# Kernel optimization log

Hardware: AMD Instinct MI355X
Metric: run time of the kernel (lower is better)

## Reference

```python
import jax, jax.numpy as jnp
import numpy as np

B, T, C, H, E, K = 8, 1024, 768, 12, 8, 2
HS = C // H          # head_size = 64
F = 4 * C            # expert hidden = 3072
DE, SE = 2, 6        # 2 'deep' experts, 6 'simple' experts (i<2 -> deep)
LN_EPS = 1e-5
TEMP_LO, TEMP_HI = 0.5, 2.0


def setup_inputs() -> dict:
    key = jax.random.key(0)
    ks = jax.random.split(key, 20)
    n = lambda k, s, sc=0.02: (jax.random.normal(k, s, dtype=jnp.float32) * sc)
    return {
        "x": jax.random.normal(ks[0], (B, T, C), dtype=jnp.float32),
        "router_noise": jax.random.normal(ks[1], (B, T, E), dtype=jnp.float32),
        # attention params (heads stacked on leading axis)
        "wq": n(ks[2], (H, C, HS)), "wk": n(ks[3], (H, C, HS)), "wv": n(ks[4], (H, C, HS)),
        "w_proj": n(ks[5], (C, C)), "b_proj": jnp.zeros((C,), jnp.float32),
        "ln1_g": jnp.ones((C,), jnp.float32), "ln1_b": jnp.zeros((C,), jnp.float32),
        "ln2_g": jnp.ones((C,), jnp.float32), "ln2_b": jnp.zeros((C,), jnp.float32),
        # router (bias init -3.0 per source)
        "w_route": n(ks[6], (C, E)), "b_route": jnp.full((E,), -3.0, jnp.float32),
        "w_noise": n(ks[7], (C, E)), "b_noise": jnp.zeros((E,), jnp.float32),
        "temperature": jnp.float32(0.8),
        # deep experts: Linear(C,4C)-GELU-Linear(4C,4C)-GELU-Linear(4C,C), residual LayerNorm
        "deep_w1": n(ks[8], (DE, C, F)), "deep_b1": jnp.zeros((DE, F), jnp.float32),
        "deep_w2": n(ks[9], (DE, F, F)), "deep_b2": jnp.zeros((DE, F), jnp.float32),
        "deep_w3": n(ks[10], (DE, F, C)), "deep_b3": jnp.zeros((DE, C), jnp.float32),
        "deep_ln_g": jnp.ones((DE, C), jnp.float32), "deep_ln_b": jnp.zeros((DE, C), jnp.float32),
        # simple experts: Linear(C,4C)-GELU-Linear(4C,C), residual LayerNorm
        "simple_w1": n(ks[11], (SE, C, F)), "simple_b1": jnp.zeros((SE, F), jnp.float32),
        "simple_w2": n(ks[12], (SE, F, C)), "simple_b2": jnp.zeros((SE, C), jnp.float32),
        "simple_ln_g": jnp.ones((SE, C), jnp.float32), "simple_ln_b": jnp.zeros((SE, C), jnp.float32),
    }


def _ln(x, g, b):
    m = jnp.mean(x, axis=-1, keepdims=True)
    v = jnp.mean((x - m) ** 2, axis=-1, keepdims=True)
    return (x - m) * jax.lax.rsqrt(v + LN_EPS) * g + b


def reference(x, router_noise, wq, wk, wv, w_proj, b_proj, ln1_g, ln1_b, ln2_g, ln2_b,
              w_route, b_route, w_noise, b_noise, temperature,
              deep_w1, deep_b1, deep_w2, deep_b2, deep_w3, deep_b3, deep_ln_g, deep_ln_b,
              simple_w1, simple_b1, simple_w2, simple_b2, simple_ln_g, simple_ln_b):
    gelu = lambda z: jax.nn.gelu(z, approximate=False)  # torch nn.GELU default = exact erf

    # ---- multi-head causal self-attention (scale = C**-0.5, full embed dim, per source) ----
    h = _ln(x, ln1_g, ln1_b)
    q = jnp.einsum('btc,hcd->bhtd', h, wq)
    k = jnp.einsum('btc,hcd->bhtd', h, wk)
    v = jnp.einsum('btc,hcd->bhtd', h, wv)
    scores = jnp.einsum('bhtd,bhsd->bhts', q, k) * (C ** -0.5)
    causal = jnp.tril(jnp.ones((T, T), dtype=bool))
    scores = jnp.where(causal, scores, -jnp.inf)
    attn = jax.nn.softmax(scores, axis=-1)
    o = jnp.einsum('bhts,bhsd->bthd', attn, v).reshape(B, T, C)
    x = x + (o @ w_proj + b_proj)

    # ---- noisy top-k router ----
    h2 = _ln(x, ln2_g, ln2_b)
    logits = h2 @ w_route + b_route                       # [B,T,E]
    noise_scale = jax.nn.softplus(h2 @ w_noise + b_noise)
    temp = jnp.clip(temperature, TEMP_LO, TEMP_HI)
    noisy = logits + temp * router_noise * noise_scale
    _, idx = jax.lax.top_k(noisy, K)                      # [B,T,K]
    mask = jnp.sum(jax.nn.one_hot(idx, E, dtype=jnp.float32), axis=-2) > 0
    gate = jax.nn.softmax(jnp.where(mask, noisy, -jnp.inf), axis=-1)  # sparse gating [B,T,E]

    # ---- dense all-expert evaluation (as in source) + gated combine ----
    N = B * T
    hf = h2.reshape(N, C)
    # deep experts (indices 0..DE-1)
    d = gelu(jnp.einsum('nc,ecf->nef', hf, deep_w1) + deep_b1)
    d = gelu(jnp.einsum('nef,efg->neg', d, deep_w2) + deep_b2)
    d = jnp.einsum('nef,efc->nec', d, deep_w3) + deep_b3
    deep_out = _ln(hf[:, None, :] + d, deep_ln_g, deep_ln_b)          # [N,DE,C]
    # simple experts (indices DE..E-1)
    s = gelu(jnp.einsum('nc,ecf->nef', hf, simple_w1) + simple_b1)
    s = jnp.einsum('nef,efc->nec', s, simple_w2) + simple_b2
    simple_out = _ln(hf[:, None, :] + s, simple_ln_g, simple_ln_b)    # [N,SE,C]

    out_all = jnp.concatenate([deep_out, simple_out], axis=1)         # [N,E,C]
    final = jnp.einsum('nec,ne->nc', out_all, gate.reshape(N, E))
    return x + final.reshape(B, T, C)
```

## Files before the change

### kernel.cpp

```cpp
#include <hip/hip_runtime.h>
#include <cstdint>
#include <cstddef>
#include <math.h>

typedef uint16_t u16;
typedef __attribute__((ext_vector_type(8))) short short8;
typedef __attribute__((ext_vector_type(4))) float f32x4;

#define TOK 8192
#define CDIM 768
#define FDIM 3072

#define GLDS16(g, l) __builtin_amdgcn_global_load_lds((const __attribute__((address_space(1))) uint32_t*)(g), (__attribute__((address_space(3))) uint32_t*)(l), 16, 0, 0)

__device__ __forceinline__ u16 f2bf(float f) {
  union { float f; uint32_t u; } v; v.f = f;
  uint32_t u = v.u;
  return (u16)((u + 0x7FFFu + ((u >> 16) & 1u)) >> 16);
}

__device__ __forceinline__ void split2(float y, u16& hi, u16& lo) {
  u16 h = f2bf(y);
  union { uint32_t u; float f; } hf; hf.u = ((uint32_t)h) << 16;
  hi = h;
  lo = f2bf(y - hf.f);
}

__device__ __forceinline__ float gelu_exact(float z) {
  return 0.5f * z * (1.0f + erff(z * 0.70710678118654752f));
}

__device__ __forceinline__ float softplus_f(float x) {
  return (x > 0.0f) ? (x + log1pf(expf(-x))) : log1pf(expf(x));
}

__device__ __forceinline__ float block_sum256(float v, float* sm) {
  #pragma unroll
  for (int m = 1; m < 64; m <<= 1) v += __shfl_xor(v, m);
  int w = threadIdx.x >> 6;
  if ((threadIdx.x & 63) == 0) sm[w] = v;
  __syncthreads();
  v = sm[0] + sm[1] + sm[2] + sm[3];
  __syncthreads();
  return v;
}


__global__ __launch_bounds__(256) void pack_qkv(const float* __restrict__ wq,
    const float* __restrict__ wk, const float* __restrict__ wv, float* __restrict__ W) {
  int id = blockIdx.x * 256 + threadIdx.x;
  if (id >= 768 * 2304) return;
  int c = id / 2304, j = id - c * 2304;
  int which = j / 768, jj = j - which * 768;
  int hh = jj >> 6, d = jj & 63;
  const float* src = (which == 0) ? wq : (which == 1 ? wk : wv);
  W[id] = src[((size_t)hh * 768 + c) * 64 + d];
}

__global__ __launch_bounds__(256) void transpose_cast(const float* __restrict__ src,
    u16* __restrict__ dst, int K, int N) {
  __shared__ float t[32][33];
  size_t eoff = (size_t)blockIdx.z * K * N;
  const float* S = src + eoff;
  u16* D = dst + eoff;
  int n0 = blockIdx.x * 32, k0 = blockIdx.y * 32;
  int tc = threadIdx.x & 31, tr = threadIdx.x >> 5;
  #pragma unroll
  for (int r = tr; r < 32; r += 8) t[r][tc] = S[(size_t)(k0 + r) * N + n0 + tc];
  __syncthreads();
  #pragma unroll
  for (int r = tr; r < 32; r += 8) D[(size_t)(n0 + r) * K + k0 + tc] = f2bf(t[tc][r]);
}

__global__ __launch_bounds__(256) void transpose_split_k(const float* __restrict__ src,
    u16* __restrict__ Dhi, u16* __restrict__ Dlo, int K, int N) {
  __shared__ float t[32][33];
  int n0 = blockIdx.x * 32, k0 = blockIdx.y * 32;
  int tc = threadIdx.x & 31, tr = threadIdx.x >> 5;
  #pragma unroll
  for (int r = tr; r < 32; r += 8) t[r][tc] = src[(size_t)(k0 + r) * N + n0 + tc];
  __syncthreads();
  #pragma unroll
  for (int r = tr; r < 32; r += 8) {
    u16 hi, lo;
    split2(t[tc][r], hi, lo);
    size_t o = (size_t)(n0 + r) * K + k0 + tc;
    Dhi[o] = hi; Dlo[o] = lo;
  }
}


__global__ __launch_bounds__(256) void ln1_split_k(const float* __restrict__ X,
    const float* __restrict__ g, const float* __restrict__ b,
    u16* __restrict__ Yhi, u16* __restrict__ Ylo) {
  __shared__ float sm[4];
  size_t row = blockIdx.x;
  const float* x = X + row * 768;
  int t = threadIdx.x;
  float v0 = x[t], v1 = x[t + 256], v2 = x[t + 512];
  float mean = block_sum256(v0 + v1 + v2, sm) * (1.0f / 768.0f);
  float d0 = v0 - mean, d1 = v1 - mean, d2 = v2 - mean;
  float var = block_sum256(d0 * d0 + d1 * d1 + d2 * d2, sm) * (1.0f / 768.0f);
  float rstd = 1.0f / sqrtf(var + 1e-5f);
  float y0 = d0 * rstd * g[t]       + b[t];
  float y1 = d1 * rstd * g[t + 256] + b[t + 256];
  float y2 = d2 * rstd * g[t + 512] + b[t + 512];
  u16 h, lo;
  split2(y0, h, lo); Yhi[row * 768 + t]       = h; Ylo[row * 768 + t]       = lo;
  split2(y1, h, lo); Yhi[row * 768 + t + 256] = h; Ylo[row * 768 + t + 256] = lo;
  split2(y2, h, lo); Yhi[row * 768 + t + 512] = h; Ylo[row * 768 + t + 512] = lo;
}

__global__ __launch_bounds__(256) void ln2_k(const float* __restrict__ X,
    const float* __restrict__ g, const float* __restrict__ b, float* __restrict__ H2,
    u16* __restrict__ H2b, float* __restrict__ OutInit) {
  __shared__ float sm[4];
  size_t row = blockIdx.x;
  const float* x = X + row * 768;
  int t = threadIdx.x;
  float v0 = x[t], v1 = x[t + 256], v2 = x[t + 512];
  float mean = block_sum256(v0 + v1 + v2, sm) * (1.0f / 768.0f);
  float d0 = v0 - mean, d1 = v1 - mean, d2 = v2 - mean;
  float var = block_sum256(d0 * d0 + d1 * d1 + d2 * d2, sm) * (1.0f / 768.0f);
  float rstd = 1.0f / sqrtf(var + 1e-5f);
  float y0 = d0 * rstd * g[t]       + b[t];
  float y1 = d1 * rstd * g[t + 256] + b[t + 256];
  float y2 = d2 * rstd * g[t + 512] + b[t + 512];
  float* h2r = H2 + row * 768;
  u16* hbr = H2b + row * 768;
  float* outr = OutInit + row * 768;
  h2r[t] = y0; h2r[t + 256] = y1; h2r[t + 512] = y2;
  hbr[t] = f2bf(y0); hbr[t + 256] = f2bf(y1); hbr[t + 512] = f2bf(y2);
  outr[t] = v0; outr[t + 256] = v1; outr[t + 512] = v2;
}


template<int BIAS_RES>
__global__ __launch_bounds__(256) void gemm_bf16x3(
    const u16* __restrict__ Ahi, const u16* __restrict__ Alo,
    const u16* __restrict__ Bhi, const u16* __restrict__ Blo,
    const float* __restrict__ bias, const float* __restrict__ Res,
    float* __restrict__ Cout, int N, int K) {
  __shared__ __align__(16) u16 Ah[128 * 32];
  __shared__ __align__(16) u16 Al[128 * 32];
  __shared__ __align__(16) u16 Bh[128 * 32];
  __shared__ __align__(16) u16 Bl[128 * 32];
  const int tid = threadIdx.x;
  const int l = tid & 63, w = tid >> 6;
  const int m0 = blockIdx.y << 7, n0 = blockIdx.x << 7;
  const int wr = w >> 1, wc = w & 1;
  f32x4 zero = {0.0f, 0.0f, 0.0f, 0.0f};
  f32x4 acc[4][4];
  #pragma unroll
  for (int mi = 0; mi < 4; mi++)
    #pragma unroll
    for (int ni = 0; ni < 4; ni++) acc[mi][ni] = zero;

  const int c0 = (w << 7) + l, c1 = c0 + 64;
  for (int k0 = 0; k0 < K; k0 += 32) {
    {
      size_t ao0 = (size_t)(m0 + (c0 >> 2)) * K + k0 + ((c0 & 3) << 3);
      size_t bo0 = (size_t)(n0 + (c0 >> 2)) * K + k0 + ((c0 & 3) << 3);
      GLDS16(Ahi + ao0, Ah + c0 * 8);
      GLDS16(Alo + ao0, Al + c0 * 8);
      GLDS16(Bhi + bo0, Bh + c0 * 8);
      GLDS16(Blo + bo0, Bl + c0 * 8);
      size_t ao1 = (size_t)(m0 + (c1 >> 2)) * K + k0 + ((c1 & 3) << 3);
      size_t bo1 = (size_t)(n0 + (c1 >> 2)) * K + k0 + ((c1 & 3) << 3);
      GLDS16(Ahi + ao1, Ah + c1 * 8);
      GLDS16(Alo + ao1, Al + c1 * 8);
      GLDS16(Bhi + bo1, Bh + c1 * 8);
      GLDS16(Blo + bo1, Bl + c1 * 8);
    }
    __syncthreads();
    short8 avh[4], avl[4], bvh[4], bvl[4];
    const int ra = (wr << 6) + (l & 15);
    const int rb = (wc << 6) + (l & 15);
    const int ko = (l >> 4) << 3;
    #pragma unroll
    for (int mi = 0; mi < 4; mi++) {
      avh[mi] = *(const short8*)(Ah + (ra + mi * 16) * 32 + ko);
      avl[mi] = *(const short8*)(Al + (ra + mi * 16) * 32 + ko);
    }
    #pragma unroll
    for (int ni = 0; ni < 4; ni++) {
      bvh[ni] = *(const short8*)(Bh + (rb + ni * 16) * 32 + ko);
      bvl[ni] = *(const short8*)(Bl + (rb + ni * 16) * 32 + ko);
    }
    #pragma unroll
    for (int mi = 0; mi < 4; mi++)
      #pragma unroll
      for (int ni = 0; ni < 4; ni++) {
        acc[mi][ni] = __builtin_amdgcn_mfma_f32_16x16x32_bf16(avl[mi], bvh[ni], acc[mi][ni], 0, 0, 0);
        acc[mi][ni] = __builtin_amdgcn_mfma_f32_16x16x32_bf16(avh[mi], bvl[ni], acc[mi][ni], 0, 0, 0);
        acc[mi][ni] = __builtin_amdgcn_mfma_f32_16x16x32_bf16(avh[mi], bvh[ni], acc[mi][ni], 0, 0, 0);
      }
    __syncthreads();
  }
  const int lr = (l >> 4) << 2;
  const int lc = l & 15;
  #pragma unroll
  for (int mi = 0; mi < 4; mi++) {
    #pragma unroll
    for (int ni = 0; ni < 4; ni++) {
      const int col = n0 + (wc << 6) + ni * 16 + lc;
      const float bv2 = BIAS_RES ? bias[col] : 0.0f;
      #pragma unroll
      for (int v = 0; v < 4; v++) {
        const size_t row = (size_t)m0 + (wr << 6) + mi * 16 + lr + v;
        float val = acc[mi][ni][v] + bv2;
        if (BIAS_RES) val += Res[row * N + col];
        Cout[row * N + col] = val;
      }
    }
  }
}


__global__ __launch_bounds__(256) void attn_k(const float* __restrict__ QKV,
    u16* __restrict__ Ohi, u16* __restrict__ Olo) {
  __shared__ __align__(16) float Qs[64 * 68];
  __shared__ __align__(16) float Ks[64 * 68];
  __shared__ __align__(16) float Vs[64 * 64];
  const int qt = (int)gridDim.x - 1 - (int)blockIdx.x;
  const int hh = blockIdx.y, bb = blockIdx.z;
  const int tid = threadIdx.x, tx = tid & 15, ty = tid >> 4;
  const int q0 = qt * 64;
  const float scale = 0.03608439182435161f;
  {
    int r = tid & 63, kg = (tid >> 6) * 16;
    const float* g = QKV + ((size_t)bb * 1024 + q0 + r) * 2304 + hh * 64 + kg;
    #pragma unroll
    for (int jj = 0; jj < 16; jj += 4) {
      float4 p = *(const float4*)(g + jj);
      Qs[(kg + jj + 0) * 68 + r] = p.x;
      Qs[(kg + jj + 1) * 68 + r] = p.y;
      Qs[(kg + jj + 2) * 68 + r] = p.z;
      Qs[(kg + jj + 3) * 68 + r] = p.w;
    }
  }
  float o[4][4] = {};
  float mrun[4], lrun[4] = {};
  #pragma unroll
  for (int i = 0; i < 4; i++) mrun[i] = -__builtin_inff();

  for (int st = 0; st <= qt; st++) {
    __syncthreads();
    {
      int r = tid & 63, kg = (tid >> 6) * 16;
      const float* g = QKV + ((size_t)bb * 1024 + st * 64 + r) * 2304 + 768 + hh * 64 + kg;
      #pragma unroll
      for (int jj = 0; jj < 16; jj += 4) {
        float4 p = *(const float4*)(g + jj);
        Ks[(kg + jj + 0) * 68 + r] = p.x;
        Ks[(kg + jj + 1) * 68 + r] = p.y;
        Ks[(kg + jj + 2) * 68 + r] = p.z;
        Ks[(kg + jj + 3) * 68 + r] = p.w;
      }
      #pragma unroll
      for (int kk = 0; kk < 4; kk++) {
        int f = tid + kk * 256;
        int s = f >> 4, j4 = (f & 15) << 2;
        *(float4*)&Vs[(s << 6) + j4] =
            *(const float4*)(QKV + ((size_t)bb * 1024 + st * 64 + s) * 2304 + 1536 + hh * 64 + j4);
      }
    }
    __syncthreads();
    float sc[4][4] = {};
    #pragma unroll 4
    for (int k = 0; k < 64; k++) {
      float4 qv = *(const float4*)&Qs[k * 68 + (ty << 2)];
      float4 kv = *(const float4*)&Ks[k * 68 + (tx << 2)];
      float qa[4] = {qv.x, qv.y, qv.z, qv.w};
      float kb[4] = {kv.x, kv.y, kv.z, kv.w};
      #pragma unroll
      for (int i = 0; i < 4; i++)
        #pragma unroll
        for (int j = 0; j < 4; j++)
          sc[i][j] = fmaf(qa[i], kb[j], sc[i][j]);
    }
    const bool diag = (st == qt);
    float mt[4];
    #pragma unroll
    for (int i = 0; i < 4; i++) {
      float mrow = -3.0e38f;
      #pragma unroll
      for (int j = 0; j < 4; j++) {
        float v = sc[i][j] * scale;
        if (diag && ((tx << 2) + j > (ty << 2) + i)) v = -__builtin_inff();
        sc[i][j] = v;
        mrow = fmaxf(mrow, v);
      }
      mt[i] = mrow;
    }
    #pragma unroll
    for (int mk = 1; mk < 16; mk <<= 1)
      #pragma unroll
      for (int i = 0; i < 4; i++) mt[i] = fmaxf(mt[i], __shfl_xor(mt[i], mk));
    float sfv[4], psum[4];
    #pragma unroll
    for (int i = 0; i < 4; i++) {
      float mnew = fmaxf(mrun[i], mt[i]);
      sfv[i] = expf(mrun[i] - mnew);
      mrun[i] = mnew;
      float rs = 0.0f;
      #pragma unroll
      for (int j = 0; j < 4; j++) {
        float pv = expf(sc[i][j] - mnew);
        sc[i][j] = pv;
        rs += pv;
      }
      psum[i] = rs;
    }
    #pragma unroll
    for (int mk = 1; mk < 16; mk <<= 1)
      #pragma unroll
      for (int i = 0; i < 4; i++) psum[i] += __shfl_xor(psum[i], mk);
    #pragma unroll
    for (int i = 0; i < 4; i++) {
      lrun[i] = lrun[i] * sfv[i] + psum[i];
      #pragma unroll
      for (int j = 0; j < 4; j++) o[i][j] *= sfv[i];
    }
    __syncthreads();
    {
      float pt[4][4];
      #pragma unroll
      for (int i = 0; i < 4; i++)
        #pragma unroll
        for (int j = 0; j < 4; j++) pt[j][i] = sc[i][j];
      #pragma unroll
      for (int j = 0; j < 4; j++)
        *(float4*)&Ks[((tx << 2) + j) * 68 + (ty << 2)] = *(const float4*)&pt[j][0];
    }
    __syncthreads();
    #pragma unroll 4
    for (int s2 = 0; s2 < 64; s2++) {
      float4 pv = *(const float4*)&Ks[s2 * 68 + (ty << 2)];
      float4 vv = *(const float4*)&Vs[(s2 << 6) + (tx << 2)];
      float pa[4] = {pv.x, pv.y, pv.z, pv.w};
      float vb4[4] = {vv.x, vv.y, vv.z, vv.w};
      #pragma unroll
      for (int i = 0; i < 4; i++)
        #pragma unroll
        for (int j = 0; j < 4; j++)
          o[i][j] = fmaf(pa[i], vb4[j], o[i][j]);
    }
  }
  #pragma unroll
  for (int i = 0; i < 4; i++) {
    float inv = 1.0f / lrun[i];
    ushort4 vh, vl;
    u16 h0, l0;
    split2(o[i][0] * inv, h0, l0); vh.x = h0; vl.x = l0;
    split2(o[i][1] * inv, h0, l0); vh.y = h0; vl.y = l0;
    split2(o[i][2] * inv, h0, l0); vh.z = h0; vl.z = l0;
    split2(o[i][3] * inv, h0, l0); vh.w = h0; vl.w = l0;
    size_t base = ((size_t)bb * 1024 + q0 + (ty << 2) + i) * 768 + hh * 64 + (tx << 2);
    *(ushort4*)&Ohi[base] = vh;
    *(ushort4*)&Olo[base] = vl;
  }
}


__global__ __launch_bounds__(256) void router_k(const float* __restrict__ h2,
    const float* __restrict__ w_route, const float* __restrict__ b_route,
    const float* __restrict__ w_noise, const float* __restrict__ b_noise,
    const float* __restrict__ rnoise, const float* __restrict__ tp, float* __restrict__ gate) {
  __shared__ float Wl[6144], Wn[6144];
  int t = threadIdx.x;
  for (int i = t; i < 1536; i += 256) {
    ((float4*)Wl)[i] = ((const float4*)w_route)[i];
    ((float4*)Wn)[i] = ((const float4*)w_noise)[i];
  }
  __syncthreads();
  int tok = blockIdx.x * 64 + (t >> 2);
  int sub = t & 3;
  const float* hr = h2 + (size_t)tok * 768;
  float aL[8] = {}, aN[8] = {};
  for (int i = 0; i < 192; i++) {
    int c = sub + (i << 2);
    float hv = hr[c];
    const float* wl = &Wl[c * 8];
    const float* wn = &Wn[c * 8];
    #pragma unroll
    for (int e = 0; e < 8; e++) { aL[e] = fmaf(hv, wl[e], aL[e]); aN[e] = fmaf(hv, wn[e], aN[e]); }
  }
  #pragma unroll
  for (int e = 0; e < 8; e++) {
    aL[e] += __shfl_xor(aL[e], 1); aL[e] += __shfl_xor(aL[e], 2);
    aN[e] += __shfl_xor(aN[e], 1); aN[e] += __shfl_xor(aN[e], 2);
  }
  if (sub == 0) {
    float temp = fminf(fmaxf(tp[0], 0.5f), 2.0f);
    float noisy[8];
    #pragma unroll
    for (int e = 0; e < 8; e++) {
      float lg = aL[e] + b_route[e];
      float ns = softplus_f(aN[e] + b_noise[e]);
      noisy[e] = lg + temp * rnoise[(size_t)tok * 8 + e] * ns;
    }
    int i1 = 0; float v1 = noisy[0];
    #pragma unroll
    for (int e = 1; e < 8; e++) if (noisy[e] > v1) { v1 = noisy[e]; i1 = e; }
    int i2 = -1; float v2 = 0.0f;
    #pragma unroll
    for (int e = 0; e < 8; e++) {
      if (e == i1) continue;
      if (i2 < 0 || noisy[e] > v2) { v2 = noisy[e]; i2 = e; }
    }
    float e2 = expf(v2 - v1);
    float denom = 1.0f + e2;
    float* gr = gate + (size_t)tok * 8;
    #pragma unroll
    for (int e = 0; e < 8; e++) gr[e] = 0.0f;
    gr[i1] = 1.0f / denom;
    gr[i2] = e2 / denom;
  }
}


__global__ void zero_counts(int* counts) {
  if (threadIdx.x < 8) counts[threadIdx.x] = 0;
}

__global__ __launch_bounds__(256) void assign_k(const float* __restrict__ gate,
    int* __restrict__ counts, int* __restrict__ idxbuf) {
  int tok = blockIdx.x * 256 + threadIdx.x;
  const float* gr = gate + (size_t)tok * 8;
  #pragma unroll
  for (int e = 0; e < 8; e++) {
    if (gr[e] > 0.0f) {
      int s = atomicAdd(&counts[e], 1);
      idxbuf[e * TOK + s] = tok;
    }
  }
}


template<int GELU_OUT, int BF16_OUT, int GATHER>
__global__ __launch_bounds__(256) void gemm_bf16_cnt(const u16* __restrict__ A,
    const u16* __restrict__ BT, const float* __restrict__ bias, void* __restrict__ Cout,
    const int* __restrict__ ridx, const int* __restrict__ cntp, int N, int K) {
  const int cnt = *cntp;
  const int mtiles = (cnt + 127) >> 7;
  if ((int)blockIdx.y >= mtiles) return;
  __shared__ __align__(16) u16 As[128 * 32];
  __shared__ __align__(16) u16 Bs[128 * 32];
  const int tid = threadIdx.x;
  const int l = tid & 63, w = tid >> 6;
  const int m0 = blockIdx.y << 7, n0 = blockIdx.x << 7;
  const int wr = w >> 1, wc = w & 1;
  const int ca = (w << 7) + l, cb = ca + 64;
  const int ra_ = m0 + (ca >> 2), rb_ = m0 + (cb >> 2);
  size_t ga, gb;
  if (GATHER) {
    ga = (size_t)ridx[ra_ < cnt ? ra_ : 0];
    gb = (size_t)ridx[rb_ < cnt ? rb_ : 0];
  } else {
    ga = (size_t)ra_; gb = (size_t)rb_;
  }
  f32x4 zero = {0.0f, 0.0f, 0.0f, 0.0f};
  f32x4 acc[4][4];
  #pragma unroll
  for (int mi = 0; mi < 4; mi++)
    #pragma unroll
    for (int ni = 0; ni < 4; ni++) acc[mi][ni] = zero;

  for (int k0 = 0; k0 < K; k0 += 32) {
    GLDS16(A + ga * K + k0 + ((ca & 3) << 3), As + ca * 8);
    GLDS16(BT + (size_t)(n0 + (ca >> 2)) * K + k0 + ((ca & 3) << 3), Bs + ca * 8);
    GLDS16(A + gb * K + k0 + ((cb & 3) << 3), As + cb * 8);
    GLDS16(BT + (size_t)(n0 + (cb >> 2)) * K + k0 + ((cb & 3) << 3), Bs + cb * 8);
    __syncthreads();
    short8 av[4], bv[4];
    const int ra = (wr << 6) + (l & 15);
    const int rb = (wc << 6) + (l & 15);
    const int ko = (l >> 4) << 3;
    #pragma unroll
    for (int mi = 0; mi < 4; mi++) av[mi] = *(const short8*)(As + (ra + mi * 16) * 32 + ko);
    #pragma unroll
    for (int ni = 0; ni < 4; ni++) bv[ni] = *(const short8*)(Bs + (rb + ni * 16) * 32 + ko);
    #pragma unroll
    for (int mi = 0; mi < 4; mi++)
      #pragma unroll
      for (int ni = 0; ni < 4; ni++)
        acc[mi][ni] = __builtin_amdgcn_mfma_f32_16x16x32_bf16(av[mi], bv[ni], acc[mi][ni], 0, 0, 0);
    __syncthreads();
  }
  const int lr = (l >> 4) << 2;
  const int lc = l & 15;
  #pragma unroll
  for (int mi = 0; mi < 4; mi++) {
    #pragma unroll
    for (int ni = 0; ni < 4; ni++) {
      const int col = n0 + (wc << 6) + ni * 16 + lc;
      const float bv2 = bias ? bias[col] : 0.0f;
      #pragma unroll
      for (int v = 0; v < 4; v++) {
        const size_t row = (size_t)m0 + (wr << 6) + mi * 16 + lr + v;
        float val = acc[mi][ni][v] + bv2;
        if (GELU_OUT) val = gelu_exact(val);
        if (BF16_OUT) ((u16*)Cout)[row * N + col] = f2bf(val);
        else          ((float*)Cout)[row * N + col] = val;
      }
    }
  }
}


__global__ __launch_bounds__(256) void combine_sc_k(const float* __restrict__ U,
    const float* __restrict__ H2, const float* __restrict__ gate,
    const int* __restrict__ ridx, const int* __restrict__ cntp,
    const float* __restrict__ g, const float* __restrict__ b,
    float* __restrict__ Out, int eidx) {
  __shared__ float sm[4];
  int pos = blockIdx.x;
  if (pos >= *cntp) return;
  size_t tok = (size_t)ridx[pos];
  float gt = gate[tok * 8 + eidx];
  int t = threadIdx.x;
  const float* h = H2 + tok * 768;
  const float* u = U + (size_t)pos * 768;
  float v0 = h[t] + u[t], v1 = h[t + 256] + u[t + 256], v2 = h[t + 512] + u[t + 512];
  float mean = block_sum256(v0 + v1 + v2, sm) * (1.0f / 768.0f);
  float d0 = v0 - mean, d1 = v1 - mean, d2 = v2 - mean;
  float var = block_sum256(d0 * d0 + d1 * d1 + d2 * d2, sm) * (1.0f / 768.0f);
  float rstd = 1.0f / sqrtf(var + 1e-5f);
  float* o = Out + tok * 768;
  o[t]       += gt * (d0 * rstd * g[t]       + b[t]);
  o[t + 256] += gt * (d1 * rstd * g[t + 256] + b[t + 256]);
  o[t + 512] += gt * (d2 * rstd * g[t + 512] + b[t + 512]);
}


extern "C" void kernel_launch(void* const* d_in, const int* in_sizes, int n_in,
                              void* d_out, int out_size, void* d_ws, size_t ws_size,
                              hipStream_t stream) {
  (void)in_sizes; (void)n_in; (void)out_size;
  const float* xin       = (const float*)d_in[0];
  const float* rnoise    = (const float*)d_in[1];
  const float* wq        = (const float*)d_in[2];
  const float* wk        = (const float*)d_in[3];
  const float* wv        = (const float*)d_in[4];
  const float* w_proj    = (const float*)d_in[5];
  const float* b_proj    = (const float*)d_in[6];
  const float* ln1_g     = (const float*)d_in[7];
  const float* ln1_b     = (const float*)d_in[8];
  const float* ln2_g     = (const float*)d_in[9];
  const float* ln2_b     = (const float*)d_in[10];
  const float* w_route   = (const float*)d_in[11];
  const float* b_route   = (const float*)d_in[12];
  const float* w_noise   = (const float*)d_in[13];
  const float* b_noise   = (const float*)d_in[14];
  const float* temp      = (const float*)d_in[15];
  const float* deep_w1   = (const float*)d_in[16];
  const float* deep_b1   = (const float*)d_in[17];
  const float* deep_w2   = (const float*)d_in[18];
  const float* deep_b2   = (const float*)d_in[19];
  const float* deep_w3   = (const float*)d_in[20];
  const float* deep_b3   = (const float*)d_in[21];
  const float* deep_ln_g = (const float*)d_in[22];
  const float* deep_ln_b = (const float*)d_in[23];
  const float* simple_w1 = (const float*)d_in[24];
  const float* simple_b1 = (const float*)d_in[25];
  const float* simple_w2 = (const float*)d_in[26];
  const float* simple_b2 = (const float*)d_in[27];
  const float* simple_ln_g = (const float*)d_in[28];
  const float* simple_ln_b = (const float*)d_in[29];

  char* ws = (char*)d_ws;
  size_t off = 0;
  auto alloc = [&](size_t bytes) -> char* {
    char* p = ws + off;
    off += (bytes + 255) & ~(size_t)255;
    return p;
  };
  float* gate = (float*)alloc((size_t)TOK * 8 * 4);
  int*   counts = (int*)alloc(8 * 4);
  int*   idxbuf = (int*)alloc(8ull * TOK * 4);
  float* h2   = (float*)alloc((size_t)TOK * CDIM * 4);
  u16*   h2b  = (u16*)  alloc((size_t)TOK * CDIM * 2);
  float* x1   = (float*)alloc((size_t)TOK * CDIM * 4);
  char*  big  = alloc((size_t)TOK * 2304 * 4 + (size_t)TOK * CDIM * 2 * 2);
  float* QKV  = (float*)big;
  float* wqkv = (float*)big;
  u16*   Ohi  = (u16*)(big + (size_t)TOK * 2304 * 4);
  u16*   Olo  = Ohi + (size_t)TOK * CDIM;
  u16*   T1c  = (u16*)big;
  u16*   T2c  = (u16*)(big + (size_t)TOK * FDIM * 2);
  float* Uc   = x1;
  u16* WqT_hi = (u16*)alloc(2304ull * CDIM * 2);
  u16* WqT_lo = (u16*)alloc(2304ull * CDIM * 2);
  u16* WpT_hi = (u16*)alloc((size_t)CDIM * CDIM * 2);
  u16* WpT_lo = (u16*)alloc((size_t)CDIM * CDIM * 2);
  u16* Hhi    = (u16*)alloc((size_t)TOK * CDIM * 2);
  u16* Hlo    = (u16*)alloc((size_t)TOK * CDIM * 2);

  size_t wsz_all = (2ull * FDIM * CDIM + 2ull * FDIM * FDIM + 2ull * CDIM * FDIM +
                    6ull * FDIM * CDIM + 6ull * CDIM * FDIM) * 2 + 16 * 256;
  bool big_ws = ws_size >= off + wsz_all;
  u16 *dW1T = nullptr, *dW2T = nullptr, *dW3T = nullptr, *sW1T = nullptr, *sW2T = nullptr, *wbuf = nullptr;
  if (big_ws) {
    dW1T = (u16*)alloc(2ull * FDIM * CDIM * 2);
    dW2T = (u16*)alloc(2ull * FDIM * FDIM * 2);
    dW3T = (u16*)alloc(2ull * CDIM * FDIM * 2);
    sW1T = (u16*)alloc(6ull * FDIM * CDIM * 2);
    sW2T = (u16*)alloc(6ull * CDIM * FDIM * 2);
  } else {
    wbuf = (u16*)alloc((size_t)FDIM * FDIM * 2);
  }

  zero_counts<<<1, 64, 0, stream>>>(counts);
  pack_qkv<<<dim3((768 * 2304 + 255) / 256), 256, 0, stream>>>(wq, wk, wv, wqkv);
  transpose_split_k<<<dim3(2304 / 32, CDIM / 32), 256, 0, stream>>>(wqkv, WqT_hi, WqT_lo, CDIM, 2304);
  transpose_split_k<<<dim3(CDIM / 32, CDIM / 32), 256, 0, stream>>>(w_proj, WpT_hi, WpT_lo, CDIM, CDIM);
  if (big_ws) {
    transpose_cast<<<dim3(FDIM / 32, CDIM / 32, 2), 256, 0, stream>>>(deep_w1, dW1T, CDIM, FDIM);
    transpose_cast<<<dim3(FDIM / 32, FDIM / 32, 2), 256, 0, stream>>>(deep_w2, dW2T, FDIM, FDIM);
    transpose_cast<<<dim3(CDIM / 32, FDIM / 32, 2), 256, 0, stream>>>(deep_w3, dW3T, FDIM, CDIM);
    transpose_cast<<<dim3(FDIM / 32, CDIM / 32, 6), 256, 0, stream>>>(simple_w1, sW1T, CDIM, FDIM);
    transpose_cast<<<dim3(CDIM / 32, FDIM / 32, 6), 256, 0, stream>>>(simple_w2, sW2T, FDIM, CDIM);
  }
  ln1_split_k<<<TOK, 256, 0, stream>>>(xin, ln1_g, ln1_b, Hhi, Hlo);
  gemm_bf16x3<0><<<dim3(2304 / 128, TOK / 128), 256, 0, stream>>>(
      Hhi, Hlo, WqT_hi, WqT_lo, nullptr, nullptr, QKV, 2304, CDIM);
  attn_k<<<dim3(16, 12, 8), 256, 0, stream>>>(QKV, Ohi, Olo);
  gemm_bf16x3<1><<<dim3(CDIM / 128, TOK / 128), 256, 0, stream>>>(
      Ohi, Olo, WpT_hi, WpT_lo, b_proj, xin, x1, CDIM, CDIM);
  ln2_k<<<TOK, 256, 0, stream>>>(x1, ln2_g, ln2_b, h2, h2b, (float*)d_out);
  router_k<<<128, 256, 0, stream>>>(h2, w_route, b_route, w_noise, b_noise, rnoise, temp, gate);
  assign_k<<<TOK / 256, 256, 0, stream>>>(gate, counts, idxbuf);

  const dim3 gF(FDIM / 128, TOK / 128);
  const dim3 gC(CDIM / 128, TOK / 128);

  for (int e = 0; e < 2; e++) {
    const int* cp = counts + e;
    const int* ri = idxbuf + e * TOK;
    const u16* W1;
    if (big_ws) W1 = dW1T + (size_t)e * FDIM * CDIM;
    else {
      transpose_cast<<<dim3(FDIM / 32, CDIM / 32, 1), 256, 0, stream>>>(deep_w1 + (size_t)e * CDIM * FDIM, wbuf, CDIM, FDIM);
      W1 = wbuf;
    }
    gemm_bf16_cnt<1, 1, 1><<<gF, 256, 0, stream>>>(h2b, W1, deep_b1 + e * FDIM, (void*)T1c, ri, cp, FDIM, CDIM);
    const u16* W2;
    if (big_ws) W2 = dW2T + (size_t)e * FDIM * FDIM;
    else {
      transpose_cast<<<dim3(FDIM / 32, FDIM / 32, 1), 256, 0, stream>>>(deep_w2 + (size_t)e * FDIM * FDIM, wbuf, FDIM, FDIM);
      W2 = wbuf;
    }
    gemm_bf16_cnt<1, 1, 0><<<gF, 256, 0, stream>>>(T1c, W2, deep_b2 + e * FDIM, (void*)T2c, ri, cp, FDIM, FDIM);
    const u16* W3;
    if (big_ws) W3 = dW3T + (size_t)e * CDIM * FDIM;
    else {
      transpose_cast<<<dim3(CDIM / 32, FDIM / 32, 1), 256, 0, stream>>>(deep_w3 + (size_t)e * FDIM * CDIM, wbuf, FDIM, CDIM);
      W3 = wbuf;
    }
    gemm_bf16_cnt<0, 0, 0><<<gC, 256, 0, stream>>>(T2c, W3, deep_b3 + e * CDIM, (void*)Uc, ri, cp, CDIM, FDIM);
    combine_sc_k<<<TOK, 256, 0, stream>>>(Uc, h2, gate, ri, cp, deep_ln_g + e * CDIM, deep_ln_b + e * CDIM, (float*)d_out, e);
  }
  for (int e = 0; e < 6; e++) {
    const int* cp = counts + 2 + e;
    const int* ri = idxbuf + (size_t)(2 + e) * TOK;
    const u16* W1;
    if (big_ws) W1 = sW1T + (size_t)e * FDIM * CDIM;
    else {
      transpose_cast<<<dim3(FDIM / 32, CDIM / 32, 1), 256, 0, stream>>>(simple_w1 + (size_t)e * CDIM * FDIM, wbuf, CDIM, FDIM);
      W1 = wbuf;
    }
    gemm_bf16_cnt<1, 1, 1><<<gF, 256, 0, stream>>>(h2b, W1, simple_b1 + e * FDIM, (void*)T1c, ri, cp, FDIM, CDIM);
    const u16* W2;
    if (big_ws) W2 = sW2T + (size_t)e * CDIM * FDIM;
    else {
      transpose_cast<<<dim3(CDIM / 32, FDIM / 32, 1), 256, 0, stream>>>(simple_w2 + (size_t)e * FDIM * CDIM, wbuf, FDIM, CDIM);
      W2 = wbuf;
    }
    gemm_bf16_cnt<0, 0, 0><<<gC, 256, 0, stream>>>(T1c, W2, simple_b2 + e * CDIM, (void*)Uc, ri, cp, CDIM, FDIM);
    combine_sc_k<<<TOK, 256, 0, stream>>>(Uc, h2, gate, ri, cp, simple_ln_g + e * CDIM, simple_ln_b + e * CDIM, (float*)d_out, 2 + e);
  }
}
```

Baseline: 2.106 ms.

## Batch simple experts into grouped GEMMs and prefetch K/V in attention

```diff
diff --git a/kernel.cpp b/kernel.cpp
--- a/kernel.cpp
+++ b/kernel.cpp
@@ -10,6 +10,8 @@
 #define TOK 8192
 #define CDIM 768
 #define FDIM 3072
+#define TOTAL_S 17152
+#define ST_MAX 134
 
 #define GLDS16(g, l) __builtin_amdgcn_global_load_lds((const __attribute__((address_space(1))) uint32_t*)(g), (__attribute__((address_space(3))) uint32_t*)(l), 16, 0, 0)
 
@@ -19,11 +21,15 @@
   return (u16)((u + 0x7FFFu + ((u >> 16) & 1u)) >> 16);
 }
 
+__device__ __forceinline__ float bf2f(u16 h) {
+  union { uint32_t u; float f; } v; v.u = ((uint32_t)h) << 16;
+  return v.f;
+}
+
 __device__ __forceinline__ void split2(float y, u16& hi, u16& lo) {
   u16 h = f2bf(y);
-  union { uint32_t u; float f; } hf; hf.u = ((uint32_t)h) << 16;
   hi = h;
-  lo = f2bf(y - hf.f);
+  lo = f2bf(y - bf2f(h));
 }
 
 __device__ __forceinline__ float gelu_exact(float z) {
@@ -227,8 +233,14 @@
   const int tid = threadIdx.x, tx = tid & 15, ty = tid >> 4;
   const int q0 = qt * 64;
   const float scale = 0.03608439182435161f;
+  const int r = tid & 63, kg = (tid >> 6) * 16;
+  int vs_[4], vj_[4];
+  #pragma unroll
+  for (int kk = 0; kk < 4; kk++) {
+    int f = tid + kk * 256;
+    vs_[kk] = f >> 4; vj_[kk] = (f & 15) << 2;
+  }
   {
-    int r = tid & 63, kg = (tid >> 6) * 16;
     const float* g = QKV + ((size_t)bb * 1024 + q0 + r) * 2304 + hh * 64 + kg;
     #pragma unroll
     for (int jj = 0; jj < 16; jj += 4) {
@@ -239,6 +251,15 @@
       Qs[(kg + jj + 3) * 68 + r] = p.w;
     }
   }
+  float4 kp[4], vp[4];
+  {
+    const float* gk = QKV + ((size_t)bb * 1024 + r) * 2304 + 768 + hh * 64 + kg;
+    #pragma unroll
+    for (int jj = 0; jj < 4; jj++) kp[jj] = *(const float4*)(gk + jj * 4);
+    #pragma unroll
+    for (int kk = 0; kk < 4; kk++)
+      vp[kk] = *(const float4*)(QKV + ((size_t)bb * 1024 + vs_[kk]) * 2304 + 1536 + hh * 64 + vj_[kk]);
+  }
   float o[4][4] = {};
   float mrun[4], lrun[4] = {};
   #pragma unroll
@@ -246,24 +267,23 @@
 
   for (int st = 0; st <= qt; st++) {
     __syncthreads();
-    {
-      int r = tid & 63, kg = (tid >> 6) * 16;
-      const float* g = QKV + ((size_t)bb * 1024 + st * 64 + r) * 2304 + 768 + hh * 64 + kg;
-      #pragma unroll
-      for (int jj = 0; jj < 16; jj += 4) {
-        float4 p = *(const float4*)(g + jj);
-        Ks[(kg + jj + 0) * 68 + r] = p.x;
-        Ks[(kg + jj + 1) * 68 + r] = p.y;
-        Ks[(kg + jj + 2) * 68 + r] = p.z;
-        Ks[(kg + jj + 3) * 68 + r] = p.w;
-      }
-      #pragma unroll
-      for (int kk = 0; kk < 4; kk++) {
-        int f = tid + kk * 256;
-        int s = f >> 4, j4 = (f & 15) << 2;
-        *(float4*)&Vs[(s << 6) + j4] =
-            *(const float4*)(QKV + ((size_t)bb * 1024 + st * 64 + s) * 2304 + 1536 + hh * 64 + j4);
-      }
+    #pragma unroll
+    for (int jj = 0; jj < 4; jj++) {
+      Ks[(kg + jj * 4 + 0) * 68 + r] = kp[jj].x;
+      Ks[(kg + jj * 4 + 1) * 68 + r] = kp[jj].y;
+      Ks[(kg + jj * 4 + 2) * 68 + r] = kp[jj].z;
+      Ks[(kg + jj * 4 + 3) * 68 + r] = kp[jj].w;
+    }
+    #pragma unroll
+    for (int kk = 0; kk < 4; kk++)
+      *(float4*)&Vs[(vs_[kk] << 6) + vj_[kk]] = vp[kk];
+    if (st < qt) {
+      const float* gk = QKV + ((size_t)bb * 1024 + (st + 1) * 64 + r) * 2304 + 768 + hh * 64 + kg;
+      #pragma unroll
+      for (int jj = 0; jj < 4; jj++) kp[jj] = *(const float4*)(gk + jj * 4);
+      #pragma unroll
+      for (int kk = 0; kk < 4; kk++)
+        vp[kk] = *(const float4*)(QKV + ((size_t)bb * 1024 + (st + 1) * 64 + vs_[kk]) * 2304 + 1536 + hh * 64 + vj_[kk]);
     }
     __syncthreads();
     float sc[4][4] = {};
@@ -435,6 +455,29 @@
       idxbuf[e * TOK + s] = tok;
     }
   }
+}
+
+__global__ void scan_k(const int* __restrict__ counts, int* __restrict__ sstart) {
+  if (threadIdx.x == 0) {
+    int acc = 0;
+    for (int j = 0; j < 6; j++) {
+      sstart[j] = acc;
+      acc += (counts[2 + j] + 127) & ~127;
+    }
+    sstart[6] = acc;
+  }
+}
+
+__global__ __launch_bounds__(256) void ridx_fill_k(const int* __restrict__ counts,
+    const int* __restrict__ sstart, const int* __restrict__ idxbuf, int* __restrict__ ridx_s) {
+  int p = blockIdx.x * 256 + threadIdx.x;
+  if (p >= sstart[6]) return;
+  int j = 0;
+  #pragma unroll
+  for (int t = 1; t < 6; t++) if (p >= sstart[t]) j = t;
+  int local = p - sstart[j];
+  if (local >= counts[2 + j]) local = 0;
+  ridx_s[p] = idxbuf[(2 + j) * TOK + local];
 }
 
 
@@ -508,6 +551,132 @@
   }
 }
 
+__global__ __launch_bounds__(256) void gemm_moe1(const u16* __restrict__ A,
+    const u16* __restrict__ W1T, const float* __restrict__ b1, u16* __restrict__ T1g,
+    const int* __restrict__ ridx_s, const int* __restrict__ sstart) {
+  const int m0 = (int)blockIdx.y << 7;
+  if (m0 >= sstart[6]) return;
+  int j = 0;
+  #pragma unroll
+  for (int t = 1; t < 6; t++) if (m0 >= sstart[t]) j = t;
+  const u16* BT = W1T + (size_t)j * FDIM * CDIM;
+  const float* bias = b1 + (size_t)j * FDIM;
+  const int N = FDIM, K = CDIM;
+  __shared__ __align__(16) u16 As[128 * 32];
+  __shared__ __align__(16) u16 Bs[128 * 32];
+  const int tid = threadIdx.x;
+  const int l = tid & 63, w = tid >> 6;
+  const int n0 = blockIdx.x << 7;
+  const int wr = w >> 1, wc = w & 1;
+  const int ca = (w << 7) + l, cb = ca + 64;
+  size_t ga = (size_t)ridx_s[m0 + (ca >> 2)];
+  size_t gb = (size_t)ridx_s[m0 + (cb >> 2)];
+  f32x4 zero = {0.0f, 0.0f, 0.0f, 0.0f};
+  f32x4 acc[4][4];
+  #pragma unroll
+  for (int mi = 0; mi < 4; mi++)
+    #pragma unroll
+    for (int ni = 0; ni < 4; ni++) acc[mi][ni] = zero;
+  for (int k0 = 0; k0 < K; k0 += 32) {
+    GLDS16(A + ga * K + k0 + ((ca & 3) << 3), As + ca * 8);
+    GLDS16(BT + (size_t)(n0 + (ca >> 2)) * K + k0 + ((ca & 3) << 3), Bs + ca * 8);
+    GLDS16(A + gb * K + k0 + ((cb & 3) << 3), As + cb * 8);
+    GLDS16(BT + (size_t)(n0 + (cb >> 2)) * K + k0 + ((cb & 3) << 3), Bs + cb * 8);
+    __syncthreads();
+    short8 av[4], bv[4];
+    const int ra = (wr << 6) + (l & 15);
+    const int rb = (wc << 6) + (l & 15);
+    const int ko = (l >> 4) << 3;
+    #pragma unroll
+    for (int mi = 0; mi < 4; mi++) av[mi] = *(const short8*)(As + (ra + mi * 16) * 32 + ko);
+    #pragma unroll
+    for (int ni = 0; ni < 4; ni++) bv[ni] = *(const short8*)(Bs + (rb + ni * 16) * 32 + ko);
+    #pragma unroll
+    for (int mi = 0; mi < 4; mi++)
+      #pragma unroll
+      for (int ni = 0; ni < 4; ni++)
+        acc[mi][ni] = __builtin_amdgcn_mfma_f32_16x16x32_bf16(av[mi], bv[ni], acc[mi][ni], 0, 0, 0);
+    __syncthreads();
+  }
+  const int lr = (l >> 4) << 2;
+  const int lc = l & 15;
+  #pragma unroll
+  for (int mi = 0; mi < 4; mi++)
+    #pragma unroll
+    for (int ni = 0; ni < 4; ni++) {
+      const int col = n0 + (wc << 6) + ni * 16 + lc;
+      const float bv2 = bias[col];
+      #pragma unroll
+      for (int v = 0; v < 4; v++) {
+        const size_t row = (size_t)m0 + (wr << 6) + mi * 16 + lr + v;
+        T1g[row * N + col] = f2bf(gelu_exact(acc[mi][ni][v] + bv2));
+      }
+    }
+}
+
+__global__ __launch_bounds__(256) void gemm_moe2(const u16* __restrict__ A,
+    const u16* __restrict__ W2T, const float* __restrict__ b2, u16* __restrict__ Us,
+    const int* __restrict__ sstart) {
+  const int m0 = (int)blockIdx.y << 7;
+  if (m0 >= sstart[6]) return;
+  int j = 0;
+  #pragma unroll
+  for (int t = 1; t < 6; t++) if (m0 >= sstart[t]) j = t;
+  const u16* BT = W2T + (size_t)j * CDIM * FDIM;
+  const float* bias = b2 + (size_t)j * CDIM;
+  const int N = CDIM, K = FDIM;
+  __shared__ __align__(16) u16 As[128 * 32];
+  __shared__ __align__(16) u16 Bs[128 * 32];
+  const int tid = threadIdx.x;
+  const int l = tid & 63, w = tid >> 6;
+  const int n0 = blockIdx.x << 7;
+  const int wr = w >> 1, wc = w & 1;
+  const int ca = (w << 7) + l, cb = ca + 64;
+  size_t ga = (size_t)(m0 + (ca >> 2));
+  size_t gb = (size_t)(m0 + (cb >> 2));
+  f32x4 zero = {0.0f, 0.0f, 0.0f, 0.0f};
+  f32x4 acc[4][4];
+  #pragma unroll
+  for (int mi = 0; mi < 4; mi++)
+    #pragma unroll
+    for (int ni = 0; ni < 4; ni++) acc[mi][ni] = zero;
+  for (int k0 = 0; k0 < K; k0 += 32) {
+    GLDS16(A + ga * K + k0 + ((ca & 3) << 3), As + ca * 8);
+    GLDS16(BT + (size_t)(n0 + (ca >> 2)) * K + k0 + ((ca & 3) << 3), Bs + ca * 8);
+    GLDS16(A + gb * K + k0 + ((cb & 3) << 3), As + cb * 8);
+    GLDS16(BT + (size_t)(n0 + (cb >> 2)) * K + k0 + ((cb & 3) << 3), Bs + cb * 8);
+    __syncthreads();
+    short8 av[4], bv[4];
+    const int ra = (wr << 6) + (l & 15);
+    const int rb = (wc << 6) + (l & 15);
+    const int ko = (l >> 4) << 3;
+    #pragma unroll
+    for (int mi = 0; mi < 4; mi++) av[mi] = *(const short8*)(As + (ra + mi * 16) * 32 + ko);
+    #pragma unroll
+    for (int ni = 0; ni < 4; ni++) bv[ni] = *(const short8*)(Bs + (rb + ni * 16) * 32 + ko);
+    #pragma unroll
+    for (int mi = 0; mi < 4; mi++)
+      #pragma unroll
+      for (int ni = 0; ni < 4; ni++)
+        acc[mi][ni] = __builtin_amdgcn_mfma_f32_16x16x32_bf16(av[mi], bv[ni], acc[mi][ni], 0, 0, 0);
+    __syncthreads();
+  }
+  const int lr = (l >> 4) << 2;
+  const int lc = l & 15;
+  #pragma unroll
+  for (int mi = 0; mi < 4; mi++)
+    #pragma unroll
+    for (int ni = 0; ni < 4; ni++) {
+      const int col = n0 + (wc << 6) + ni * 16 + lc;
+      const float bv2 = bias[col];
+      #pragma unroll
+      for (int v = 0; v < 4; v++) {
+        const size_t row = (size_t)m0 + (wr << 6) + mi * 16 + lr + v;
+        Us[row * N + col] = f2bf(acc[mi][ni][v] + bv2);
+      }
+    }
+}
+
 
 __global__ __launch_bounds__(256) void combine_sc_k(const float* __restrict__ U,
     const float* __restrict__ H2, const float* __restrict__ gate,
@@ -523,6 +692,37 @@
   const float* h = H2 + tok * 768;
   const float* u = U + (size_t)pos * 768;
   float v0 = h[t] + u[t], v1 = h[t + 256] + u[t + 256], v2 = h[t + 512] + u[t + 512];
+  float mean = block_sum256(v0 + v1 + v2, sm) * (1.0f / 768.0f);
+  float d0 = v0 - mean, d1 = v1 - mean, d2 = v2 - mean;
+  float var = block_sum256(d0 * d0 + d1 * d1 + d2 * d2, sm) * (1.0f / 768.0f);
+  float rstd = 1.0f / sqrtf(var + 1e-5f);
+  float* o = Out + tok * 768;
+  o[t]       += gt * (d0 * rstd * g[t]       + b[t]);
+  o[t + 256] += gt * (d1 * rstd * g[t + 256] + b[t + 256]);
+  o[t + 512] += gt * (d2 * rstd * g[t + 512] + b[t + 512]);
+}
+
+__global__ __launch_bounds__(256) void combine_s_k(const u16* __restrict__ Us,
+    const float* __restrict__ H2, const float* __restrict__ gate,
+    const int* __restrict__ ridx_s, const int* __restrict__ counts, const int* __restrict__ sstart,
+    const float* __restrict__ sg, const float* __restrict__ sb, float* __restrict__ Out) {
+  __shared__ float sm[4];
+  int p = blockIdx.x;
+  if (p >= sstart[6]) return;
+  int j = 0;
+  #pragma unroll
+  for (int t2 = 1; t2 < 6; t2++) if (p >= sstart[t2]) j = t2;
+  if (p - sstart[j] >= counts[2 + j]) return;
+  size_t tok = (size_t)ridx_s[p];
+  float gt = gate[tok * 8 + 2 + j];
+  int t = threadIdx.x;
+  const float* h = H2 + tok * 768;
+  const u16* u = Us + (size_t)p * 768;
+  const float* g = sg + (size_t)j * 768;
+  const float* b = sb + (size_t)j * 768;
+  float v0 = h[t] + bf2f(u[t]);
+  float v1 = h[t + 256] + bf2f(u[t + 256]);
+  float v2 = h[t + 512] + bf2f(u[t + 512]);
   float mean = block_sum256(v0 + v1 + v2, sm) * (1.0f / 768.0f);
   float d0 = v0 - mean, d1 = v1 - mean, d2 = v2 - mean;
   float var = block_sum256(d0 * d0 + d1 * d1 + d2 * d2, sm) * (1.0f / 768.0f);
@@ -578,17 +778,22 @@
   };
   float* gate = (float*)alloc((size_t)TOK * 8 * 4);
   int*   counts = (int*)alloc(8 * 4);
+  int*   sstart = (int*)alloc(8 * 4);
   int*   idxbuf = (int*)alloc(8ull * TOK * 4);
+  int*   ridx_s = (int*)alloc((size_t)TOTAL_S * 4);
   float* h2   = (float*)alloc((size_t)TOK * CDIM * 4);
   u16*   h2b  = (u16*)  alloc((size_t)TOK * CDIM * 2);
   float* x1   = (float*)alloc((size_t)TOK * CDIM * 4);
-  char*  big  = alloc((size_t)TOK * 2304 * 4 + (size_t)TOK * CDIM * 2 * 2);
+  size_t big_a = (size_t)TOK * 2304 * 4 + (size_t)TOK * CDIM * 2 * 2;
+  size_t big_b = (size_t)TOTAL_S * FDIM * 2;
+  char*  big  = alloc(big_a > big_b ? big_a : big_b);
   float* QKV  = (float*)big;
   float* wqkv = (float*)big;
   u16*   Ohi  = (u16*)(big + (size_t)TOK * 2304 * 4);
   u16*   Olo  = Ohi + (size_t)TOK * CDIM;
   u16*   T1c  = (u16*)big;
   u16*   T2c  = (u16*)(big + (size_t)TOK * FDIM * 2);
+  u16*   T1g  = (u16*)big;
   float* Uc   = x1;
   u16* WqT_hi = (u16*)alloc(2304ull * CDIM * 2);
   u16* WqT_lo = (u16*)alloc(2304ull * CDIM * 2);
@@ -596,6 +801,7 @@
   u16* WpT_lo = (u16*)alloc((size_t)CDIM * CDIM * 2);
   u16* Hhi    = (u16*)alloc((size_t)TOK * CDIM * 2);
   u16* Hlo    = (u16*)alloc((size_t)TOK * CDIM * 2);
+  u16* Us = WqT_hi;
 
   size_t wsz_all = (2ull * FDIM * CDIM + 2ull * FDIM * FDIM + 2ull * CDIM * FDIM +
                     6ull * FDIM * CDIM + 6ull * CDIM * FDIM) * 2 + 16 * 256;
@@ -631,6 +837,8 @@
   ln2_k<<<TOK, 256, 0, stream>>>(x1, ln2_g, ln2_b, h2, h2b, (float*)d_out);
   router_k<<<128, 256, 0, stream>>>(h2, w_route, b_route, w_noise, b_noise, rnoise, temp, gate);
   assign_k<<<TOK / 256, 256, 0, stream>>>(gate, counts, idxbuf);
+  scan_k<<<1, 64, 0, stream>>>(counts, sstart);
+  ridx_fill_k<<<(TOTAL_S + 255) / 256, 256, 0, stream>>>(counts, sstart, idxbuf, ridx_s);
 
   const dim3 gF(FDIM / 128, TOK / 128);
   const dim3 gC(CDIM / 128, TOK / 128);
@@ -661,23 +869,21 @@
     gemm_bf16_cnt<0, 0, 0><<<gC, 256, 0, stream>>>(T2c, W3, deep_b3 + e * CDIM, (void*)Uc, ri, cp, CDIM, FDIM);
     combine_sc_k<<<TOK, 256, 0, stream>>>(Uc, h2, gate, ri, cp, deep_ln_g + e * CDIM, deep_ln_b + e * CDIM, (float*)d_out, e);
   }
-  for (int e = 0; e < 6; e++) {
-    const int* cp = counts + 2 + e;
-    const int* ri = idxbuf + (size_t)(2 + e) * TOK;
-    const u16* W1;
-    if (big_ws) W1 = sW1T + (size_t)e * FDIM * CDIM;
-    else {
+
+  if (big_ws) {
+    gemm_moe1<<<dim3(FDIM / 128, ST_MAX), 256, 0, stream>>>(h2b, sW1T, simple_b1, T1g, ridx_s, sstart);
+    gemm_moe2<<<dim3(CDIM / 128, ST_MAX), 256, 0, stream>>>(T1g, sW2T, simple_b2, Us, sstart);
+    combine_s_k<<<TOTAL_S, 256, 0, stream>>>(Us, h2, gate, ridx_s, counts, sstart,
+                                             simple_ln_g, simple_ln_b, (float*)d_out);
+  } else {
+    for (int e = 0; e < 6; e++) {
+      const int* cp = counts + 2 + e;
+      const int* ri = idxbuf + (size_t)(2 + e) * TOK;
       transpose_cast<<<dim3(FDIM / 32, CDIM / 32, 1), 256, 0, stream>>>(simple_w1 + (size_t)e * CDIM * FDIM, wbuf, CDIM, FDIM);
-      W1 = wbuf;
-    }
-    gemm_bf16_cnt<1, 1, 1><<<gF, 256, 0, stream>>>(h2b, W1, simple_b1 + e * FDIM, (void*)T1c, ri, cp, FDIM, CDIM);
-    const u16* W2;
-    if (big_ws) W2 = sW2T + (size_t)e * CDIM * FDIM;
-    else {
+      gemm_bf16_cnt<1, 1, 1><<<gF, 256, 0, stream>>>(h2b, wbuf, simple_b1 + e * FDIM, (void*)T1c, ri, cp, FDIM, CDIM);
       transpose_cast<<<dim3(CDIM / 32, FDIM / 32, 1), 256, 0, stream>>>(simple_w2 + (size_t)e * FDIM * CDIM, wbuf, FDIM, CDIM);
-      W2 = wbuf;
-    }
-    gemm_bf16_cnt<0, 0, 0><<<gC, 256, 0, stream>>>(T1c, W2, simple_b2 + e * CDIM, (void*)Uc, ri, cp, CDIM, FDIM);
-    combine_sc_k<<<TOK, 256, 0, stream>>>(Uc, h2, gate, ri, cp, simple_ln_g + e * CDIM, simple_ln_b + e * CDIM, (float*)d_out, 2 + e);
-  }
-}
+      gemm_bf16_cnt<0, 0, 0><<<gC, 256, 0, stream>>>(T1c, wbuf, simple_b2 + e * CDIM, (void*)Uc, ri, cp, CDIM, FDIM);
+      combine_sc_k<<<TOK, 256, 0, stream>>>(Uc, h2, gate, ri, cp, simple_ln_g + e * CDIM, simple_ln_b + e * CDIM, (float*)d_out, 2 + e);
+    }
+  }
+}
```

Measured after the change: 2.060 ms. 1.02x faster.
